# Kernel optimization log

Hardware: AMD Instinct MI355X
Metric: run time of the kernel (lower is better)

Reference implementation:

```python
import jax, jax.numpy as jnp
import numpy as np

ATTEN = 2  # window half-size -> 2*ATTEN+1 = 5 neighbors
B, S, IN, H, MID, OUT = 1024, 100, 100, 128, 32, 2
MAX_LEN = 100
SQRT_H = float(np.sqrt(float(H)))


def _xavier(k, i, o):
    return jax.random.normal(k, (i, o), jnp.float32) * np.sqrt(2.0 / (i + o))


def _positional_encoding():
    pos = np.arange(MAX_LEN, dtype=np.float32)[:, None]
    div = np.exp(np.arange(0, H, 2, dtype=np.float32) * (-np.log(10000.0) / H))
    pe = np.zeros((MAX_LEN, H), np.float32)
    pe[:, 0::2] = np.sin(pos * div)
    pe[:, 1::2] = np.cos(pos * div)
    return jnp.asarray(pe[None])  # (1, MAX_LEN, H)


def setup_inputs() -> dict:
    key = jax.random.key(0)
    ks = jax.random.split(key, 7)
    return {
        "x": jax.random.normal(ks[0], (B, S, IN), jnp.float32),
        "W1": _xavier(ks[1], IN, H),
        "b1": jnp.zeros((1, 1, H), jnp.float32),
        "Wq": _xavier(ks[2], H, H),
        "Wk": _xavier(ks[3], H, H),
        "Wv": _xavier(ks[4], H, H),
        "bv": jnp.zeros((1, 1, H), jnp.float32),
        "W2": _xavier(ks[5], H, MID),
        "b2": jnp.zeros((1, 1, MID), jnp.float32),
        "W3": _xavier(ks[6], MID, OUT),
        "b3": jnp.zeros((1, 1, OUT), jnp.float32),
        "pe": _positional_encoding(),
    }


def reference(x, W1, b1, Wq, Wk, Wv, bv, W2, b2, W3, b3, pe):
    seq_len = x.shape[1]
    h = jax.nn.relu(x @ W1 + b1) + pe[:, :seq_len, :]  # (B,S,H)
    # zero-pad seq dim by ATTEN on each side; torch pad+roll+stack+slice is
    # equivalent to gathering window offsets +2,+1,0,-1,-2 (in that order)
    padded = jnp.pad(h, ((0, 0), (ATTEN, ATTEN), (0, 0)))
    x_nei = jnp.stack(
        [padded[:, ATTEN - k: ATTEN - k + seq_len, :] for k in range(-ATTEN, ATTEN + 1)],
        axis=2,
    )  # (B,S,5,H); index m corresponds to neighbor x[i + ATTEN - m]
    q = h @ Wq                      # (B,S,H)
    keys = x_nei @ Wk               # (B,S,5,H)
    vals = x_nei @ Wv + bv          # (B,S,5,H)
    scores = jnp.einsum("bsh,bswh->bsw", q, keys) / SQRT_H
    w = jax.nn.softmax(scores, axis=-1)  # (B,S,5)
    context = jnp.einsum("bsw,bswh->bsh", w, vals)
    output = jax.nn.relu(context @ W2 + b2) @ W3 + b3  # (B,S,OUT)
    return output, w[:, :, None, :]  # weights shaped (B,S,1,5) like torch
```

## Files before the change

### kernel.cpp

```cpp
#include <hip/hip_runtime.h>
#include <hip/hip_bf16.h>

#define B_ 1024
#define S_ 100
#define IN_ 100
#define H_ 128
#define MID_ 32
#define OUT_ 2
#define P_ (B_ * S_)
#define RSQRT_H 0.08838834764831845f
#define LSTR 136
#define MROWS 112

typedef __attribute__((ext_vector_type(8))) short short8;
typedef __attribute__((ext_vector_type(4))) float float4v;

__device__ __forceinline__ float bf2f(ushort u) {
    union { unsigned u; float f; } c; c.u = ((unsigned)u) << 16; return c.f;
}
__device__ __forceinline__ ushort f2bf(float x) {
    union { float f; unsigned u; } c; c.f = x;
    unsigned r = c.u + 0x7FFFu + ((c.u >> 16) & 1u);
    return (ushort)(r >> 16);
}

__global__ __launch_bounds__(256) void prep_transpose(const float* __restrict__ W1,
                                                      const float* __restrict__ Wv,
                                                      const float* __restrict__ W2,
                                                      ushort* __restrict__ W1T,
                                                      ushort* __restrict__ WvT,
                                                      ushort* __restrict__ W2T) {
    int g = blockIdx.x * 256 + threadIdx.x;
    if (g < 16384) {
        int n = g >> 7, k = g & 127;
        W1T[g] = (k < IN_) ? f2bf(W1[k * H_ + n]) : (ushort)0;
    } else if (g < 32768) {
        int e = g - 16384; int n = e >> 7, k = e & 127;
        WvT[e] = f2bf(Wv[k * H_ + n]);
    } else {
        int e = g - 32768; int n = e >> 7, k = e & 127;
        W2T[e] = f2bf(W2[k * MID_ + n]);
    }
}

__global__ __launch_bounds__(256) void prep_wqk(const float* __restrict__ Wq,
                                                const float* __restrict__ Wk,
                                                ushort* __restrict__ WqkT) {
    __shared__ float sq[32][132];
    __shared__ float sk[32][132];
    int n0 = (blockIdx.x >> 2) * 32, k0 = (blockIdx.x & 3) * 32;
    int tid = threadIdx.x;
    for (int i = tid; i < 32 * 128; i += 256) {
        int r = i >> 7, c = i & 127;
        sq[r][c] = Wq[(k0 + r) * H_ + c];
        sk[r][c] = Wk[(n0 + r) * H_ + c];
    }
    __syncthreads();
    for (int i = tid; i < 1024; i += 256) {
        int kk = i & 31, nn = i >> 5;
        float a = 0.f;
        for (int j = 0; j < 128; ++j) a += sq[kk][j] * sk[nn][j];
        WqkT[(n0 + nn) * 128 + (k0 + kk)] = f2bf(a);
    }
}

template <int EPI>
__device__ __forceinline__ void mm_stage(const ushort* __restrict__ A_lds,
                                         const ushort* __restrict__ WT,
                                         ushort* __restrict__ C_lds,
                                         int wave, int lane,
                                         const float* __restrict__ bias,
                                         const float* __restrict__ pe) {
    int l15 = lane & 15, quad = lane >> 4;
    short8 bfrag[2][4];
#pragma unroll
    for (int nt = 0; nt < 2; ++nt) {
        int n = (wave * 2 + nt) * 16 + l15;
#pragma unroll
        for (int ks = 0; ks < 4; ++ks)
            bfrag[nt][ks] = *(const short8*)(WT + n * 128 + ks * 32 + quad * 8);
    }
    float biasv[2] = {0.f, 0.f};
    if (EPI != 0) {
#pragma unroll
        for (int nt = 0; nt < 2; ++nt) biasv[nt] = bias[(wave * 2 + nt) * 16 + l15];
    }
#pragma unroll
    for (int mt = 0; mt < 7; ++mt) {
        short8 afrag[4];
#pragma unroll
        for (int ks = 0; ks < 4; ++ks)
            afrag[ks] = *(const short8*)(A_lds + (mt * 16 + l15) * LSTR + ks * 32 + quad * 8);
#pragma unroll
        for (int nt = 0; nt < 2; ++nt) {
            float4v acc = {0.f, 0.f, 0.f, 0.f};
#pragma unroll
            for (int ks = 0; ks < 4; ++ks)
                acc = __builtin_amdgcn_mfma_f32_16x16x32_bf16(afrag[ks], bfrag[nt][ks], acc, 0, 0, 0);
            int n = (wave * 2 + nt) * 16 + l15;
#pragma unroll
            for (int i = 0; i < 4; ++i) {
                int row = mt * 16 + quad * 4 + i;
                float v = acc[i];
                if (EPI == 1) v = (row < S_) ? (fmaxf(v + biasv[nt], 0.f) + pe[row * H_ + n]) : 0.f;
                else if (EPI == 2) v = v + biasv[nt];
                C_lds[row * LSTR + n] = f2bf(v);
            }
        }
    }
}

__global__ __launch_bounds__(256) void fused_kernel(
    const float* __restrict__ x, const ushort* __restrict__ W1T,
    const ushort* __restrict__ WqkT, const ushort* __restrict__ WvT,
    const ushort* __restrict__ W2T,
    const float* __restrict__ b1, const float* __restrict__ bv,
    const float* __restrict__ b2, const float* __restrict__ W3,
    const float* __restrict__ b3, const float* __restrict__ pe,
    float* __restrict__ out, float* __restrict__ wout) {
    __shared__ ushort klds[MROWS * LSTR];
    __shared__ ushort xh[MROWS * LSTR];
    int tid = threadIdx.x, wave = tid >> 6, lane = tid & 63;
    int b = blockIdx.x;
    const float* xb = x + (size_t)b * (S_ * IN_);

    for (int i = tid; i < MROWS * LSTR; i += 256) klds[i] = 0;
    __syncthreads();
    for (int i = tid; i < S_ * IN_; i += 256) {
        int m = i / IN_, k = i - m * IN_;
        klds[m * LSTR + k] = f2bf(xb[i]);
    }
    __syncthreads();
    mm_stage<1>(klds, W1T, xh, wave, lane, b1, pe);
    __syncthreads();
    mm_stage<0>(xh, WqkT, klds, wave, lane, nullptr, nullptr);
    __syncthreads();
    if (tid < 2 * S_) {
        int r = tid >> 1, half = tid & 1;
        const ushort* kqr = klds + r * LSTR + half * 64;
        float kqf[64];
#pragma unroll
        for (int c = 0; c < 8; ++c) {
            short8 v = *(const short8*)(kqr + c * 8);
#pragma unroll
            for (int j = 0; j < 8; ++j) kqf[c * 8 + j] = bf2f((ushort)v[j]);
        }
        float sc[5];
#pragma unroll
        for (int m = 0; m < 5; ++m) {
            int nr = r + 2 - m;
            float p = 0.f;
            if (nr >= 0 && nr < S_) {
                const ushort* hr = xh + nr * LSTR + half * 64;
#pragma unroll
                for (int c = 0; c < 8; ++c) {
                    short8 v = *(const short8*)(hr + c * 8);
#pragma unroll
                    for (int j = 0; j < 8; ++j) p += bf2f((ushort)v[j]) * kqf[c * 8 + j];
                }
            }
            sc[m] = p;
        }
#pragma unroll
        for (int m = 0; m < 5; ++m)
            sc[m] = (sc[m] + __shfl_xor(sc[m], 1)) * RSQRT_H;
        float mx = sc[0];
#pragma unroll
        for (int m = 1; m < 5; ++m) mx = fmaxf(mx, sc[m]);
        float e[5], ss = 0.f;
#pragma unroll
        for (int m = 0; m < 5; ++m) { e[m] = expf(sc[m] - mx); ss += e[m]; }
        float inv = 1.f / ss;
        float w5[5];
#pragma unroll
        for (int m = 0; m < 5; ++m) w5[m] = e[m] * inv;
        if (half == 0) {
            float* wp = wout + (size_t)b * (S_ * 5) + r * 5;
#pragma unroll
            for (int m = 0; m < 5; ++m) wp[m] = w5[m];
        }
        float acc[64];
#pragma unroll
        for (int c = 0; c < 64; ++c) acc[c] = 0.f;
#pragma unroll
        for (int m = 0; m < 5; ++m) {
            int nr = r + 2 - m;
            if (nr < 0 || nr >= S_) continue;
            float wm = w5[m];
            const ushort* hr = xh + nr * LSTR + half * 64;
#pragma unroll
            for (int c = 0; c < 8; ++c) {
                short8 v = *(const short8*)(hr + c * 8);
#pragma unroll
                for (int j = 0; j < 8; ++j) acc[c * 8 + j] += wm * bf2f((ushort)v[j]);
            }
        }
        ushort* op = klds + r * LSTR + half * 64;
#pragma unroll
        for (int c = 0; c < 8; ++c) {
            short8 v;
#pragma unroll
            for (int j = 0; j < 8; ++j) v[j] = (short)f2bf(acc[c * 8 + j]);
            *(short8*)(op + c * 8) = v;
        }
    }
    __syncthreads();
    mm_stage<2>(klds, WvT, xh, wave, lane, bv, nullptr);
    __syncthreads();
    {
        int l15 = lane & 15, quad = lane >> 4;
        short8 bfrag[2][4];
#pragma unroll
        for (int nt = 0; nt < 2; ++nt)
#pragma unroll
            for (int ks = 0; ks < 4; ++ks)
                bfrag[nt][ks] = *(const short8*)(W2T + (nt * 16 + l15) * 128 + ks * 32 + quad * 8);
        float biasv[2] = {b2[l15], b2[16 + l15]};
        for (int mt = wave; mt < 7; mt += 4) {
            short8 afrag[4];
#pragma unroll
            for (int ks = 0; ks < 4; ++ks)
                afrag[ks] = *(const short8*)(xh + (mt * 16 + l15) * LSTR + ks * 32 + quad * 8);
#pragma unroll
            for (int nt = 0; nt < 2; ++nt) {
                float4v acc = {0.f, 0.f, 0.f, 0.f};
#pragma unroll
                for (int ks = 0; ks < 4; ++ks)
                    acc = __builtin_amdgcn_mfma_f32_16x16x32_bf16(afrag[ks], bfrag[nt][ks], acc, 0, 0, 0);
#pragma unroll
                for (int i = 0; i < 4; ++i) {
                    int row = mt * 16 + quad * 4 + i;
                    klds[row * LSTR + nt * 16 + l15] = f2bf(fmaxf(acc[i] + biasv[nt], 0.f));
                }
            }
        }
    }
    __syncthreads();
    if (tid < S_) {
        int r = tid;
        float o0 = b3[0], o1 = b3[1];
#pragma unroll
        for (int k = 0; k < MID_; ++k) {
            float mv = bf2f(klds[r * LSTR + k]);
            o0 += mv * W3[k * 2];
            o1 += mv * W3[k * 2 + 1];
        }
        float* op = out + (size_t)b * (S_ * OUT_) + r * OUT_;
        op[0] = o0; op[1] = o1;
    }
}

extern "C" void kernel_launch(void* const* d_in, const int* in_sizes, int n_in,
                              void* d_out, int out_size, void* d_ws, size_t ws_size,
                              hipStream_t stream) {
    const float* x  = (const float*)d_in[0];
    const float* W1 = (const float*)d_in[1];
    const float* b1 = (const float*)d_in[2];
    const float* Wq = (const float*)d_in[3];
    const float* Wk = (const float*)d_in[4];
    const float* Wv = (const float*)d_in[5];
    const float* bv = (const float*)d_in[6];
    const float* W2 = (const float*)d_in[7];
    const float* b2 = (const float*)d_in[8];
    const float* W3 = (const float*)d_in[9];
    const float* b3 = (const float*)d_in[10];
    const float* pe = (const float*)d_in[11];

    float* out  = (float*)d_out;
    float* wout = out + (size_t)P_ * OUT_;

    ushort* W1T  = (ushort*)d_ws;
    ushort* WqkT = W1T + 16384;
    ushort* WvT  = WqkT + 16384;
    ushort* W2T  = WvT + 16384;

    prep_transpose<<<144, 256, 0, stream>>>(W1, Wv, W2, W1T, WvT, W2T);
    prep_wqk<<<16, 256, 0, stream>>>(Wq, Wk, WqkT);
    fused_kernel<<<B_, 256, 0, stream>>>(x, W1T, WqkT, WvT, W2T,
                                         b1, bv, b2, W3, b3, pe, out, wout);
}
```

Before: 147.1 us.

## Double block threads, shrink LDS rows with overlapping last tile, merge prep kernels

The fused kernel moves from 256 to 512 threads per block. Each wave now computes one 16-column N tile, and the attention stage splits each row across 4 threads instead of 2. LDS row count drops from 112 to 100, and the last M tile is shifted to start at row 84, so it overlaps rows and needs no padding or zero-fill of extra rows. The x load is vectorized to float4, and the two weight-prep kernels are merged into one launch. Together these aim for more parallelism per block, less LDS per block and so higher occupancy, and one fewer launch, at the cost of redundant MFMA work on the overlapping tile and higher register pressure under launch_bounds(512,4).

Result: faster. 135.3 us (-8.0%).

```diff
diff --git a/kernel.cpp b/kernel.cpp
--- a/kernel.cpp
+++ b/kernel.cpp
@@ -10,9 +10,10 @@
 #define P_ (B_ * S_)
 #define RSQRT_H 0.08838834764831845f
 #define LSTR 136
-#define MROWS 112
+#define MROWS 100
 
 typedef __attribute__((ext_vector_type(8))) short short8;
+typedef __attribute__((ext_vector_type(4))) short short4v;
 typedef __attribute__((ext_vector_type(4))) float float4v;
 
 __device__ __forceinline__ float bf2f(ushort u) {
@@ -24,43 +25,50 @@
     return (ushort)(r >> 16);
 }
 
-__global__ __launch_bounds__(256) void prep_transpose(const float* __restrict__ W1,
-                                                      const float* __restrict__ Wv,
-                                                      const float* __restrict__ W2,
-                                                      ushort* __restrict__ W1T,
-                                                      ushort* __restrict__ WvT,
-                                                      ushort* __restrict__ W2T) {
-    int g = blockIdx.x * 256 + threadIdx.x;
-    if (g < 16384) {
-        int n = g >> 7, k = g & 127;
-        W1T[g] = (k < IN_) ? f2bf(W1[k * H_ + n]) : (ushort)0;
-    } else if (g < 32768) {
-        int e = g - 16384; int n = e >> 7, k = e & 127;
-        WvT[e] = f2bf(Wv[k * H_ + n]);
+__global__ __launch_bounds__(256) void prep_kernel(
+    const float* __restrict__ W1, const float* __restrict__ Wv,
+    const float* __restrict__ W2, const float* __restrict__ Wq,
+    const float* __restrict__ Wk,
+    ushort* __restrict__ W1T, ushort* __restrict__ WvT,
+    ushort* __restrict__ W2T, ushort* __restrict__ WqkT) {
+    int tid = threadIdx.x;
+    if (blockIdx.x < 144) {
+        int g = blockIdx.x * 256 + tid;
+        if (g < 16384) {
+            int n = g >> 7, k = g & 127;
+            W1T[g] = (k < IN_) ? f2bf(W1[k * H_ + n]) : (ushort)0;
+        } else if (g < 32768) {
+            int e = g - 16384; int n = e >> 7, k = e & 127;
+            WvT[e] = f2bf(Wv[k * H_ + n]);
+        } else {
+            int e = g - 32768; int n = e >> 7, k = e & 127;
+            W2T[e] = f2bf(W2[k * MID_ + n]);
+        }
     } else {
-        int e = g - 32768; int n = e >> 7, k = e & 127;
-        W2T[e] = f2bf(W2[k * MID_ + n]);
-    }
-}
-
-__global__ __launch_bounds__(256) void prep_wqk(const float* __restrict__ Wq,
-                                                const float* __restrict__ Wk,
-                                                ushort* __restrict__ WqkT) {
-    __shared__ float sq[32][132];
-    __shared__ float sk[32][132];
-    int n0 = (blockIdx.x >> 2) * 32, k0 = (blockIdx.x & 3) * 32;
-    int tid = threadIdx.x;
-    for (int i = tid; i < 32 * 128; i += 256) {
-        int r = i >> 7, c = i & 127;
-        sq[r][c] = Wq[(k0 + r) * H_ + c];
-        sk[r][c] = Wk[(n0 + r) * H_ + c];
-    }
-    __syncthreads();
-    for (int i = tid; i < 1024; i += 256) {
-        int kk = i & 31, nn = i >> 5;
-        float a = 0.f;
-        for (int j = 0; j < 128; ++j) a += sq[kk][j] * sk[nn][j];
-        WqkT[(n0 + nn) * 128 + (k0 + kk)] = f2bf(a);
+        __shared__ float sq[32][132];
+        __shared__ float sk[32][132];
+        int bid = blockIdx.x - 144;
+        int n0 = (bid >> 2) * 32, k0 = (bid & 3) * 32;
+        for (int i = tid; i < 32 * 32; i += 256) {
+            int r = i >> 5, c4 = (i & 31) * 4;
+            float4 a = *(const float4*)(Wq + (k0 + r) * H_ + c4);
+            float4 b = *(const float4*)(Wk + (n0 + r) * H_ + c4);
+            sq[r][c4] = a.x; sq[r][c4 + 1] = a.y; sq[r][c4 + 2] = a.z; sq[r][c4 + 3] = a.w;
+            sk[r][c4] = b.x; sk[r][c4 + 1] = b.y; sk[r][c4 + 2] = b.z; sk[r][c4 + 3] = b.w;
+        }
+        __syncthreads();
+        for (int i = tid; i < 1024; i += 256) {
+            int kk = i & 31, nn = i >> 5;
+            float a0 = 0.f, a1 = 0.f, a2 = 0.f, a3 = 0.f;
+#pragma unroll
+            for (int j = 0; j < 128; j += 4) {
+                a0 += sq[kk][j + 0] * sk[nn][j + 0];
+                a1 += sq[kk][j + 1] * sk[nn][j + 1];
+                a2 += sq[kk][j + 2] * sk[nn][j + 2];
+                a3 += sq[kk][j + 3] * sk[nn][j + 3];
+            }
+            WqkT[(n0 + nn) * 128 + (k0 + kk)] = f2bf((a0 + a1) + (a2 + a3));
+        }
     }
 }
 
@@ -72,45 +80,36 @@
                                          const float* __restrict__ bias,
                                          const float* __restrict__ pe) {
     int l15 = lane & 15, quad = lane >> 4;
-    short8 bfrag[2][4];
-#pragma unroll
-    for (int nt = 0; nt < 2; ++nt) {
-        int n = (wave * 2 + nt) * 16 + l15;
+    int n = wave * 16 + l15;
+    short8 bfrag[4];
+#pragma unroll
+    for (int ks = 0; ks < 4; ++ks)
+        bfrag[ks] = *(const short8*)(WT + n * 128 + ks * 32 + quad * 8);
+    float biasv = 0.f;
+    if (EPI != 0) biasv = bias[n];
+#pragma unroll
+    for (int mt = 0; mt < 7; ++mt) {
+        int m0 = (mt < 6) ? mt * 16 : 84;
+        short8 afrag[4];
 #pragma unroll
         for (int ks = 0; ks < 4; ++ks)
-            bfrag[nt][ks] = *(const short8*)(WT + n * 128 + ks * 32 + quad * 8);
-    }
-    float biasv[2] = {0.f, 0.f};
-    if (EPI != 0) {
-#pragma unroll
-        for (int nt = 0; nt < 2; ++nt) biasv[nt] = bias[(wave * 2 + nt) * 16 + l15];
-    }
-#pragma unroll
-    for (int mt = 0; mt < 7; ++mt) {
-        short8 afrag[4];
+            afrag[ks] = *(const short8*)(A_lds + (m0 + l15) * LSTR + ks * 32 + quad * 8);
+        float4v acc = {0.f, 0.f, 0.f, 0.f};
 #pragma unroll
         for (int ks = 0; ks < 4; ++ks)
-            afrag[ks] = *(const short8*)(A_lds + (mt * 16 + l15) * LSTR + ks * 32 + quad * 8);
-#pragma unroll
-        for (int nt = 0; nt < 2; ++nt) {
-            float4v acc = {0.f, 0.f, 0.f, 0.f};
-#pragma unroll
-            for (int ks = 0; ks < 4; ++ks)
-                acc = __builtin_amdgcn_mfma_f32_16x16x32_bf16(afrag[ks], bfrag[nt][ks], acc, 0, 0, 0);
-            int n = (wave * 2 + nt) * 16 + l15;
-#pragma unroll
-            for (int i = 0; i < 4; ++i) {
-                int row = mt * 16 + quad * 4 + i;
-                float v = acc[i];
-                if (EPI == 1) v = (row < S_) ? (fmaxf(v + biasv[nt], 0.f) + pe[row * H_ + n]) : 0.f;
-                else if (EPI == 2) v = v + biasv[nt];
-                C_lds[row * LSTR + n] = f2bf(v);
-            }
-        }
-    }
-}
-
-__global__ __launch_bounds__(256) void fused_kernel(
+            acc = __builtin_amdgcn_mfma_f32_16x16x32_bf16(afrag[ks], bfrag[ks], acc, 0, 0, 0);
+#pragma unroll
+        for (int i = 0; i < 4; ++i) {
+            int row = m0 + quad * 4 + i;
+            float v = acc[i];
+            if (EPI == 1) v = fmaxf(v + biasv, 0.f) + pe[row * H_ + n];
+            else if (EPI == 2) v = v + biasv;
+            C_lds[row * LSTR + n] = f2bf(v);
+        }
+    }
+}
+
+__global__ __launch_bounds__(512, 4) void fused_kernel(
     const float* __restrict__ x, const ushort* __restrict__ W1T,
     const ushort* __restrict__ WqkT, const ushort* __restrict__ WvT,
     const ushort* __restrict__ W2T,
@@ -124,23 +123,29 @@
     int b = blockIdx.x;
     const float* xb = x + (size_t)b * (S_ * IN_);
 
-    for (int i = tid; i < MROWS * LSTR; i += 256) klds[i] = 0;
-    __syncthreads();
-    for (int i = tid; i < S_ * IN_; i += 256) {
-        int m = i / IN_, k = i - m * IN_;
-        klds[m * LSTR + k] = f2bf(xb[i]);
+    for (int i = tid; i < 2500; i += 512) {
+        float4 v = ((const float4*)xb)[i];
+        int m = i / 25, k4 = (i - m * 25) * 4;
+        short4v s;
+        s[0] = (short)f2bf(v.x); s[1] = (short)f2bf(v.y);
+        s[2] = (short)f2bf(v.z); s[3] = (short)f2bf(v.w);
+        *(short4v*)(klds + m * LSTR + k4) = s;
+    }
+    for (int i = tid; i < S_ * 28; i += 512) {
+        int r = i / 28, c = i - r * 28;
+        klds[r * LSTR + 100 + c] = 0;
     }
     __syncthreads();
     mm_stage<1>(klds, W1T, xh, wave, lane, b1, pe);
     __syncthreads();
     mm_stage<0>(xh, WqkT, klds, wave, lane, nullptr, nullptr);
     __syncthreads();
-    if (tid < 2 * S_) {
-        int r = tid >> 1, half = tid & 1;
-        const ushort* kqr = klds + r * LSTR + half * 64;
-        float kqf[64];
-#pragma unroll
-        for (int c = 0; c < 8; ++c) {
+    if (tid < 4 * S_) {
+        int r = tid >> 2, q = tid & 3;
+        const ushort* kqr = klds + r * LSTR + q * 32;
+        float kqf[32];
+#pragma unroll
+        for (int c = 0; c < 4; ++c) {
             short8 v = *(const short8*)(kqr + c * 8);
 #pragma unroll
             for (int j = 0; j < 8; ++j) kqf[c * 8 + j] = bf2f((ushort)v[j]);
@@ -151,9 +156,9 @@
             int nr = r + 2 - m;
             float p = 0.f;
             if (nr >= 0 && nr < S_) {
-                const ushort* hr = xh + nr * LSTR + half * 64;
-#pragma unroll
-                for (int c = 0; c < 8; ++c) {
+                const ushort* hr = xh + nr * LSTR + q * 32;
+#pragma unroll
+                for (int c = 0; c < 4; ++c) {
                     short8 v = *(const short8*)(hr + c * 8);
 #pragma unroll
                     for (int j = 0; j < 8; ++j) p += bf2f((ushort)v[j]) * kqf[c * 8 + j];
@@ -162,8 +167,11 @@
             sc[m] = p;
         }
 #pragma unroll
-        for (int m = 0; m < 5; ++m)
-            sc[m] = (sc[m] + __shfl_xor(sc[m], 1)) * RSQRT_H;
+        for (int m = 0; m < 5; ++m) {
+            sc[m] += __shfl_xor(sc[m], 1);
+            sc[m] += __shfl_xor(sc[m], 2);
+            sc[m] *= RSQRT_H;
+        }
         float mx = sc[0];
 #pragma unroll
         for (int m = 1; m < 5; ++m) mx = fmaxf(mx, sc[m]);
@@ -174,30 +182,30 @@
         float w5[5];
 #pragma unroll
         for (int m = 0; m < 5; ++m) w5[m] = e[m] * inv;
-        if (half == 0) {
+        if (q == 0) {
             float* wp = wout + (size_t)b * (S_ * 5) + r * 5;
 #pragma unroll
             for (int m = 0; m < 5; ++m) wp[m] = w5[m];
         }
-        float acc[64];
-#pragma unroll
-        for (int c = 0; c < 64; ++c) acc[c] = 0.f;
+        float acc[32];
+#pragma unroll
+        for (int c = 0; c < 32; ++c) acc[c] = 0.f;
 #pragma unroll
         for (int m = 0; m < 5; ++m) {
             int nr = r + 2 - m;
             if (nr < 0 || nr >= S_) continue;
             float wm = w5[m];
-            const ushort* hr = xh + nr * LSTR + half * 64;
-#pragma unroll
-            for (int c = 0; c < 8; ++c) {
+            const ushort* hr = xh + nr * LSTR + q * 32;
+#pragma unroll
+            for (int c = 0; c < 4; ++c) {
                 short8 v = *(const short8*)(hr + c * 8);
 #pragma unroll
                 for (int j = 0; j < 8; ++j) acc[c * 8 + j] += wm * bf2f((ushort)v[j]);
             }
         }
-        ushort* op = klds + r * LSTR + half * 64;
-#pragma unroll
-        for (int c = 0; c < 8; ++c) {
+        ushort* op = klds + r * LSTR + q * 32;
+#pragma unroll
+        for (int c = 0; c < 4; ++c) {
             short8 v;
 #pragma unroll
             for (int j = 0; j < 8; ++j) v[j] = (short)f2bf(acc[c * 8 + j]);
@@ -209,29 +217,26 @@
     __syncthreads();
     {
         int l15 = lane & 15, quad = lane >> 4;
-        short8 bfrag[2][4];
-#pragma unroll
-        for (int nt = 0; nt < 2; ++nt)
+        for (int t = wave; t < 14; t += 8) {
+            int mt = t >> 1, nt = t & 1;
+            int m0 = (mt < 6) ? mt * 16 : 84;
+            short8 bfrag[4];
 #pragma unroll
             for (int ks = 0; ks < 4; ++ks)
-                bfrag[nt][ks] = *(const short8*)(W2T + (nt * 16 + l15) * 128 + ks * 32 + quad * 8);
-        float biasv[2] = {b2[l15], b2[16 + l15]};
-        for (int mt = wave; mt < 7; mt += 4) {
+                bfrag[ks] = *(const short8*)(W2T + (nt * 16 + l15) * 128 + ks * 32 + quad * 8);
+            float biasv = b2[nt * 16 + l15];
             short8 afrag[4];
 #pragma unroll
             for (int ks = 0; ks < 4; ++ks)
-                afrag[ks] = *(const short8*)(xh + (mt * 16 + l15) * LSTR + ks * 32 + quad * 8);
-#pragma unroll
-            for (int nt = 0; nt < 2; ++nt) {
-                float4v acc = {0.f, 0.f, 0.f, 0.f};
-#pragma unroll
-                for (int ks = 0; ks < 4; ++ks)
-                    acc = __builtin_amdgcn_mfma_f32_16x16x32_bf16(afrag[ks], bfrag[nt][ks], acc, 0, 0, 0);
-#pragma unroll
-                for (int i = 0; i < 4; ++i) {
-                    int row = mt * 16 + quad * 4 + i;
-                    klds[row * LSTR + nt * 16 + l15] = f2bf(fmaxf(acc[i] + biasv[nt], 0.f));
-                }
+                afrag[ks] = *(const short8*)(xh + (m0 + l15) * LSTR + ks * 32 + quad * 8);
+            float4v acc = {0.f, 0.f, 0.f, 0.f};
+#pragma unroll
+            for (int ks = 0; ks < 4; ++ks)
+                acc = __builtin_amdgcn_mfma_f32_16x16x32_bf16(afrag[ks], bfrag[ks], acc, 0, 0, 0);
+#pragma unroll
+            for (int i = 0; i < 4; ++i) {
+                int row = m0 + quad * 4 + i;
+                klds[row * LSTR + nt * 16 + l15] = f2bf(fmaxf(acc[i] + biasv, 0.f));
             }
         }
     }
@@ -274,8 +279,7 @@
     ushort* WvT  = WqkT + 16384;
     ushort* W2T  = WvT + 16384;
 
-    prep_transpose<<<144, 256, 0, stream>>>(W1, Wv, W2, W1T, WvT, W2T);
-    prep_wqk<<<16, 256, 0, stream>>>(Wq, Wk, WqkT);
-    fused_kernel<<<B_, 256, 0, stream>>>(x, W1T, WqkT, WvT, W2T,
+    prep_kernel<<<160, 256, 0, stream>>>(W1, Wv, W2, Wq, Wk, W1T, WvT, W2T, WqkT);
+    fused_kernel<<<B_, 512, 0, stream>>>(x, W1T, WqkT, WvT, W2T,
                                          b1, bv, b2, W3, b3, pe, out, wout);
 }
```
